# Kernel optimization log

Hardware: AMD Instinct MI355X
Metric: run time of the kernel (lower is better)

Reference implementation:

```python
import jax, jax.numpy as jnp
import numpy as np

NUM_HEADS = 16


def setup_inputs() -> dict:
    key = jax.random.key(0)
    ks = jax.random.split(key, 6)
    B, S, E = 2, 2048, 1024
    scale = 1.0 / np.sqrt(E)
    return {
        "x": jax.random.normal(ks[0], (B, S, E), dtype=jnp.float32),
        "mask": jnp.ones((B, S), dtype=jnp.int32),
        "Wq": jax.random.normal(ks[1], (E, E), dtype=jnp.float32) * scale,
        "bq": jnp.zeros((E,), dtype=jnp.float32),
        "Wk": jax.random.normal(ks[2], (E, E), dtype=jnp.float32) * scale,
        "bk": jnp.zeros((E,), dtype=jnp.float32),
        "Wv": jax.random.normal(ks[3], (E, E), dtype=jnp.float32) * scale,
        "bv": jnp.zeros((E,), dtype=jnp.float32),
        "Wo": jax.random.normal(ks[4], (E, E), dtype=jnp.float32) * scale,
        "bo": jnp.zeros((E,), dtype=jnp.float32),
    }


def reference(x, mask, Wq, bq, Wk, bk, Wv, bv, Wo, bo):
    B, S, E = x.shape
    H = NUM_HEADS
    D = E // H

    def heads(t):  # [B,S,E] -> [B,H,S,D]
        return t.reshape(B, S, H, D).transpose(0, 2, 1, 3)

    q = heads(x @ Wq + bq)
    k = heads(x @ Wk + bk)
    v = heads(x @ Wv + bv)

    # scaled dot-product scores [B,H,S,S]
    scores = jnp.einsum("bhsd,bhtd->bhst", q, k) / jnp.sqrt(jnp.float32(D))
    m = mask.astype(jnp.float32)[:, None, None, :]  # key-side padding mask
    scores = scores + (-1e9) * (1.0 - m)
    weights = jax.nn.softmax(scores, axis=-1)
    attn = jnp.einsum("bhst,bhtd->bhsd", weights, v)

    concat = attn.transpose(0, 2, 1, 3).reshape(B, S, E)
    return concat @ Wo + bo
```

## Files before the change

kernel.cpp:

```cpp
#include <hip/hip_runtime.h>
#include <stdint.h>

#define E_DIM   1024
#define HNUM    16
#define DH      64
#define BATCH   2
#define SEQ     2048
#define M_TOT   (BATCH*SEQ)
#define LOG2E   1.44269504088896340736f

typedef __bf16 bf16x8 __attribute__((ext_vector_type(8)));
typedef __bf16 bf16x4 __attribute__((ext_vector_type(4)));
typedef float  f32x4  __attribute__((ext_vector_type(4)));
typedef float  f32x16 __attribute__((ext_vector_type(16)));
typedef unsigned short u16;
typedef unsigned int   u32;
typedef unsigned long long u64;
typedef u16 u16x8 __attribute__((ext_vector_type(8)));
typedef u32 u32x2 __attribute__((ext_vector_type(2)));

__device__ __forceinline__ u16 f2bf(float f) {
    u32 u = __builtin_bit_cast(u32, f);
    u32 r = 0x7FFFu + ((u >> 16) & 1u);
    return (u16)((u + r) >> 16);
}

__device__ __forceinline__ void gload_lds16(const u16* g, u16* l) {
    __builtin_amdgcn_global_load_lds(
        (const __attribute__((address_space(1))) u32*)g,
        (__attribute__((address_space(3))) u32*)l, 16, 0, 0);
}

#define MFMA16(a,b,c) __builtin_amdgcn_mfma_f32_16x16x32_bf16((a),(b),(c),0,0,0)
#define MFMA32(a,b,c) __builtin_amdgcn_mfma_f32_32x32x16_bf16((a),(b),(c),0,0,0)

__global__ __launch_bounds__(256) void cast_x_kernel(const float* __restrict__ x,
                                                     u16* __restrict__ out, int n) {
    int idx = (blockIdx.x * 256 + threadIdx.x) * 4;
    if (idx < n) {
        float4 v = *reinterpret_cast<const float4*>(x + idx);
        ushort4 o;
        o.x = f2bf(v.x); o.y = f2bf(v.y); o.z = f2bf(v.z); o.w = f2bf(v.w);
        *reinterpret_cast<ushort4*>(out + idx) = o;
    }
}

__global__ __launch_bounds__(256) void maskbits_kernel(const int* __restrict__ mask,
                                                       u64* __restrict__ bits) {
    int i = blockIdx.x * 256 + threadIdx.x;
    u64 bl = __ballot(mask[i] != 0);
    if ((i & 63) == 0) bits[i >> 6] = bl;
}

__global__ void wtrans_kernel(const float* __restrict__ w0, const float* __restrict__ w1,
                              const float* __restrict__ w2, const float* __restrict__ w3,
                              u16* __restrict__ out) {
    __shared__ float tile[32][33];
    const float* w = blockIdx.z == 0 ? w0 : blockIdx.z == 1 ? w1 : blockIdx.z == 2 ? w2 : w3;
    const int n0 = blockIdx.x * 32, k0 = blockIdx.y * 32;
    #pragma unroll
    for (int j = 0; j < 4; j++) {
        int k = k0 + threadIdx.y + j * 8;
        tile[threadIdx.y + j * 8][threadIdx.x] = w[(size_t)k * E_DIM + n0 + threadIdx.x];
    }
    __syncthreads();
    u16* o = out + (size_t)blockIdx.z * E_DIM * E_DIM;
    #pragma unroll
    for (int j = 0; j < 4; j++) {
        int n = n0 + threadIdx.y + j * 8;
        o[(size_t)n * E_DIM + k0 + threadIdx.x] = f2bf(tile[threadIdx.x][threadIdx.y + j * 8]);
    }
}

template <typename OutT>
__global__ __launch_bounds__(256) void gemm_kernel(
    const u16* __restrict__ A, const u16* __restrict__ Bt_base, OutT* __restrict__ C_base,
    const float* __restrict__ bias0, const float* __restrict__ bias1,
    const float* __restrict__ bias2, float scale0, int Mdim) {
    const int z = blockIdx.z;
    const u16* Bt = Bt_base + (size_t)z * E_DIM * E_DIM;
    OutT* C = C_base + (size_t)z * Mdim * E_DIM;
    const float* bias = (z == 0) ? bias0 : (z == 1 ? bias1 : bias2);
    const float scale = (z == 0) ? scale0 : 1.0f;

    __shared__ __align__(16) u16 Als[128 * 32];
    __shared__ __align__(16) u16 Bls[128 * 32];

    const int tid = threadIdx.x;
    const int lane = tid & 63;
    const int w = tid >> 6;
    const int wr = (w >> 1) * 64, wc = (w & 1) * 64;
    const int tm = blockIdx.y * 128, tn = blockIdx.x * 128;
    const int r4 = tid >> 2;
    const int c8 = (tid & 3) * 8;

    f32x4 acc[4][4] = {};

    for (int k0 = 0; k0 < E_DIM; k0 += 32) {
        gload_lds16(A + (size_t)(tm + r4) * E_DIM + k0 + c8, Als + tid * 8);
        gload_lds16(A + (size_t)(tm + 64 + r4) * E_DIM + k0 + c8, Als + 2048 + tid * 8);
        gload_lds16(Bt + (size_t)(tn + r4) * E_DIM + k0 + c8, Bls + tid * 8);
        gload_lds16(Bt + (size_t)(tn + 64 + r4) * E_DIM + k0 + c8, Bls + 2048 + tid * 8);
        __syncthreads();
        const int lr = lane & 15, lg = lane >> 4;
        bf16x8 af[4], bfr[4];
        #pragma unroll
        for (int m = 0; m < 4; m++)
            af[m] = *reinterpret_cast<const bf16x8*>(Als + (wr + m * 16 + lr) * 32 + lg * 8);
        #pragma unroll
        for (int n = 0; n < 4; n++)
            bfr[n] = *reinterpret_cast<const bf16x8*>(Bls + (wc + n * 16 + lr) * 32 + lg * 8);
        #pragma unroll
        for (int m = 0; m < 4; m++)
            #pragma unroll
            for (int n = 0; n < 4; n++)
                acc[m][n] = MFMA16(af[m], bfr[n], acc[m][n]);
        __syncthreads();
    }

    const int lr = lane & 15, lg = lane >> 4;
    #pragma unroll
    for (int m = 0; m < 4; m++) {
        #pragma unroll
        for (int n = 0; n < 4; n++) {
            const int col = tn + wc + n * 16 + lr;
            const float bv = bias[col];
            #pragma unroll
            for (int r = 0; r < 4; r++) {
                const int row = tm + wr + m * 16 + lg * 4 + r;
                float v = (acc[m][n][r] + bv) * scale;
                if constexpr (sizeof(OutT) == 2) {
                    C[(size_t)row * E_DIM + col] = f2bf(v);
                } else {
                    C[(size_t)row * E_DIM + col] = v;
                }
            }
        }
    }
}

__global__ __launch_bounds__(256) void attn_kernel(
    const u16* __restrict__ Q, const u16* __restrict__ K, const u16* __restrict__ V,
    const u64* __restrict__ mbits, u16* __restrict__ PO, float* __restrict__ lws) {
    __shared__ __align__(16) u16 Kls[4][64 * 64];
    __shared__ __align__(16) u16 Vt[2][64 * 64];

    const int tid = threadIdx.x;
    const int lane = tid & 63;
    const int w = tid >> 6;
    const int hi = lane >> 5;
    const int l31 = lane & 31;
    const int n = blockIdx.x;
    const int g = n & 63, qt = n >> 6;
    const int h = g & 15, zz = g >> 4;
    const int b = zz >> 1, half = zz & 1;

    const int qrow = b * SEQ + qt * 128 + w * 32 + l31;
    bf16x8 qf[4];
    #pragma unroll
    for (int kc = 0; kc < 4; kc++)
        qf[kc] = *reinterpret_cast<const bf16x8*>(Q + (size_t)qrow * E_DIM + h * DH + kc * 16 + hi * 8);

    const int krow = (l31 & 3) | ((l31 & 4) << 1) | ((l31 & 8) >> 1) | (l31 & 16);
    const u32 ksw = (u32)(krow & 7) << 4;

    const int krA = tid >> 3;
    const int kcA = (tid & 7) ^ (krA & 7);
    const size_t kgoffA = (size_t)krA * E_DIM + kcA * 8;
    const size_t kgoffB = kgoffA + (size_t)32 * E_DIM;

    const int vc = tid & 7;
    const int vsg = ((tid >> 3) ^ (vc << 2)) & 31;
    const size_t vgoff = (size_t)(2 * vsg) * E_DIM + vc * 8;

    f32x16 oacc0 = {}, oacc1 = {};
    float l_run = 0.f;

    const u16* Kg = K + (size_t)(b * SEQ + half * (SEQ / 2)) * E_DIM + h * DH;
    const u16* Vg = V + (size_t)(b * SEQ + half * (SEQ / 2)) * E_DIM + h * DH;
    const int NT = SEQ / 2 / 64;

    {
        u16x8 a0 = __builtin_bit_cast(u16x8, *reinterpret_cast<const bf16x8*>(Vg + vgoff));
        u16x8 a1 = __builtin_bit_cast(u16x8, *reinterpret_cast<const bf16x8*>(Vg + vgoff + E_DIM));
        gload_lds16(Kg + kgoffA, &Kls[0][tid * 8]);
        gload_lds16(Kg + kgoffB, &Kls[0][(tid + 256) * 8]);
        gload_lds16(Kg + (size_t)64 * E_DIM + kgoffA, &Kls[1][tid * 8]);
        gload_lds16(Kg + (size_t)64 * E_DIM + kgoffB, &Kls[1][(tid + 256) * 8]);
        #pragma unroll
        for (int j = 0; j < 8; j++) {
            const u32 off = (((u32)(vc * 8 + j) * 128) + (u32)vsg * 4) ^ ((u32)j << 4);
            *(u32*)((char*)Vt[0] + off) = (u32)a0[j] | ((u32)a1[j] << 16);
        }
        asm volatile("s_waitcnt vmcnt(2)" ::: "memory");
        asm volatile("s_waitcnt lgkmcnt(0)" ::: "memory");
        __builtin_amdgcn_sched_barrier(0);
        __builtin_amdgcn_s_barrier();
    }

    for (int kt = 0; kt < NT; kt++) {
        u16x8 a0, a1;
        if (kt + 1 < NT) {
            const u16* vg = Vg + (size_t)(kt + 1) * 64 * E_DIM;
            a0 = __builtin_bit_cast(u16x8, *reinterpret_cast<const bf16x8*>(vg + vgoff));
            a1 = __builtin_bit_cast(u16x8, *reinterpret_cast<const bf16x8*>(vg + vgoff + E_DIM));
        }
        if (kt + 2 < NT) {
            const u16* kg = Kg + (size_t)(kt + 2) * 64 * E_DIM;
            gload_lds16(kg + kgoffA, &Kls[(kt + 2) & 3][tid * 8]);
            gload_lds16(kg + kgoffB, &Kls[(kt + 2) & 3][(tid + 256) * 8]);
        }

        const char* Kb = (const char*)Kls[kt & 3];
        const char* Vb = (const char*)Vt[kt & 1];
        const u64 mb = mbits[b * (SEQ / 64) + half * NT + kt];
        float sum = 0.f;

        #pragma unroll
        for (int kh = 0; kh < 2; kh++) {
            f32x16 s = {};
            __builtin_amdgcn_s_setprio(1);
            #pragma unroll
            for (int kc = 0; kc < 4; kc++) {
                const u32 off = ((((u32)krow * 128) + (u32)kc * 32 + (u32)hi * 16) ^ ksw)
                                + (u32)kh * 4096;
                bf16x8 kf = *(const bf16x8*)(Kb + off);
                s = MFMA32(kf, qf[kc], s);
            }
            __builtin_amdgcn_s_setprio(0);
            if (mb != ~0ull) {
                #pragma unroll
                for (int r = 0; r < 16; r++) {
                    const int key = 32 * kh + (r & 3) + 4 * ((r >> 2) & 1) + 8 * hi
                                    + 16 * ((r >> 3) & 1);
                    if (!((mb >> key) & 1)) s[r] += -1.442695e9f;
                }
            }
            #pragma unroll
            for (int r = 0; r < 16; r++) { s[r] = exp2f(s[r]); sum += s[r]; }
            bf16x8 pf0, pf1;
            #pragma unroll
            for (int e = 0; e < 8; e++) { pf0[e] = (__bf16)s[e]; pf1[e] = (__bf16)s[8 + e]; }
            __builtin_amdgcn_s_setprio(1);
            #pragma unroll
            for (int kp = 0; kp < 2; kp++) {
                const int kc = 2 * kh + kp;
                const u32 roff = (((u32)l31 * 128) + (u32)(2 * kc + hi) * 16)
                                 ^ ((u32)(l31 & 7) << 4);
                bf16x8 vf0 = *(const bf16x8*)(Vb + roff);
                bf16x8 vf1 = *(const bf16x8*)(Vb + roff + 4096);
                const bf16x8 pfx = kp ? pf1 : pf0;
                oacc0 = MFMA32(vf0, pfx, oacc0);
                oacc1 = MFMA32(vf1, pfx, oacc1);
            }
            __builtin_amdgcn_s_setprio(0);
        }
        l_run += sum;

        asm volatile("s_waitcnt vmcnt(2)" ::: "memory");
        __builtin_amdgcn_sched_barrier(0);
        if (kt + 1 < NT) {
            #pragma unroll
            for (int j = 0; j < 8; j++) {
                const u32 off = (((u32)(vc * 8 + j) * 128) + (u32)vsg * 4) ^ ((u32)j << 4);
                *(u32*)((char*)Vt[(kt + 1) & 1] + off) = (u32)a0[j] | ((u32)a1[j] << 16);
            }
        }
        asm volatile("s_waitcnt lgkmcnt(0)" ::: "memory");
        __builtin_amdgcn_sched_barrier(0);
        __builtin_amdgcn_s_barrier();
    }

    const float l_tot = l_run + __shfl_xor(l_run, 32);
    u16* op = PO + ((size_t)half * M_TOT + qrow) * E_DIM + h * DH;
    #pragma unroll
    for (int db = 0; db < 2; db++) {
        #pragma unroll
        for (int j = 0; j < 4; j++) {
            bf16x4 pk;
            #pragma unroll
            for (int c = 0; c < 4; c++)
                pk[c] = (__bf16)(db ? oacc1[4 * j + c] : oacc0[4 * j + c]);
            const int d0 = 32 * db + 8 * j + 4 * hi;
            *reinterpret_cast<u32x2*>(op + d0) = __builtin_bit_cast(u32x2, pk);
        }
    }
    if (hi == 0) lws[((size_t)half * M_TOT + qrow) * HNUM + h] = l_tot;
}

__global__ __launch_bounds__(256) void combine_kernel(const u16* __restrict__ PO,
                                                      const float* __restrict__ lws,
                                                      u16* __restrict__ ab) {
    const int i = (blockIdx.x * 256 + threadIdx.x) * 8;
    const int row = i >> 10;
    const int h = (i & 1023) >> 6;
    const float l0 = lws[(size_t)row * HNUM + h];
    const float l1 = lws[((size_t)M_TOT + row) * HNUM + h];
    const float rl = 1.0f / (l0 + l1);
    const bf16x8 a = *reinterpret_cast<const bf16x8*>(PO + i);
    const bf16x8 c = *reinterpret_cast<const bf16x8*>(PO + (size_t)M_TOT * E_DIM + i);
    u16x8 o;
    #pragma unroll
    for (int j = 0; j < 8; j++)
        o[j] = f2bf(((float)a[j] + (float)c[j]) * rl);
    *reinterpret_cast<u16x8*>(ab + i) = o;
}

extern "C" void kernel_launch(void* const* d_in, const int* in_sizes, int n_in,
                              void* d_out, int out_size, void* d_ws, size_t ws_size,
                              hipStream_t stream) {
    const float* x  = (const float*)d_in[0];
    const int* mask = (const int*)d_in[1];
    const float* Wq = (const float*)d_in[2];
    const float* bq = (const float*)d_in[3];
    const float* Wk = (const float*)d_in[4];
    const float* bk = (const float*)d_in[5];
    const float* Wv = (const float*)d_in[6];
    const float* bv = (const float*)d_in[7];
    const float* Wo = (const float*)d_in[8];
    const float* bo = (const float*)d_in[9];
    float* out = (float*)d_out;

    u16* ws  = (u16*)d_ws;
    const size_t ME = (size_t)M_TOT * E_DIM;
    u16* xb  = ws;
    u16* wt  = ws + ME;
    u16* qb  = ws + 2 * ME;
    u16* kbf = ws + 3 * ME;
    u16* vbf = ws + 4 * ME;
    u64* mbf = (u64*)(ws + 5 * ME);
    float* lws = (float*)(ws + 5 * ME + 8192);
    u16* ab  = xb;
    u16* po  = (u16*)d_out;

    cast_x_kernel<<<dim3(M_TOT * E_DIM / 1024), dim3(256), 0, stream>>>(x, xb, M_TOT * E_DIM);
    wtrans_kernel<<<dim3(E_DIM / 32, E_DIM / 32, 4), dim3(32, 8), 0, stream>>>(Wq, Wk, Wv, Wo, wt);
    maskbits_kernel<<<dim3(M_TOT / 256), dim3(256), 0, stream>>>(mask, mbf);
    gemm_kernel<u16><<<dim3(E_DIM / 128, M_TOT / 128, 3), dim3(256), 0, stream>>>(
        xb, wt, qb, bq, bk, bv, 0.125f * LOG2E, M_TOT);
    attn_kernel<<<dim3(1024), dim3(256), 0, stream>>>(qb, kbf, vbf, mbf, po, lws);
    combine_kernel<<<dim3(M_TOT * E_DIM / 2048), dim3(256), 0, stream>>>(po, lws, ab);
    gemm_kernel<float><<<dim3(E_DIM / 128, M_TOT / 128, 1), dim3(256), 0, stream>>>(
        ab, wt + (size_t)3 * E_DIM * E_DIM, out, bo, bo, bo, 1.0f, M_TOT);
}
```

Before: 150.5 us.

## Software-pipeline QK^T one tile ahead and deepen K prefetch in attention

Restructures the attention loop so the QK^T MFMAs for the next key tile are issued while softmax exp and PV MFMAs for the current tile run. This overlaps the exp/convert latency with matrix work. K prefetch depth grows from two to three tiles ahead. The change also precomputes the LDS offsets, uses the v_cvt_pk_bf16_f32 packed conversion and the raw exp2 builtin, and transposes V with perm instructions. The cost is higher register pressure from the extra score accumulators.

```diff
diff --git a/kernel.cpp b/kernel.cpp
--- a/kernel.cpp
+++ b/kernel.cpp
@@ -18,6 +18,7 @@
 typedef unsigned long long u64;
 typedef u16 u16x8 __attribute__((ext_vector_type(8)));
 typedef u32 u32x2 __attribute__((ext_vector_type(2)));
+typedef u32 u32x4 __attribute__((ext_vector_type(4)));
 
 __device__ __forceinline__ u16 f2bf(float f) {
     u32 u = __builtin_bit_cast(u32, f);
@@ -29,6 +30,12 @@
     __builtin_amdgcn_global_load_lds(
         (const __attribute__((address_space(1))) u32*)g,
         (__attribute__((address_space(3))) u32*)l, 16, 0, 0);
+}
+
+__device__ __forceinline__ u32 cvt_pk_bf16(float lo, float hi) {
+    u32 r;
+    asm("v_cvt_pk_bf16_f32 %0, %1, %2" : "=v"(r) : "v"(lo), "v"(hi));
+    return r;
 }
 
 #define MFMA16(a,b,c) __builtin_amdgcn_mfma_f32_16x16x32_bf16((a),(b),(c),0,0,0)
@@ -163,6 +170,10 @@
 
     const int krow = (l31 & 3) | ((l31 & 4) << 1) | ((l31 & 8) >> 1) | (l31 & 16);
     const u32 ksw = (u32)(krow & 7) << 4;
+    u32 koff[4];
+    #pragma unroll
+    for (int kc = 0; kc < 4; kc++)
+        koff[kc] = (((u32)krow * 128) + (u32)kc * 32 + (u32)hi * 16) ^ ksw;
 
     const int krA = tid >> 3;
     const int kcA = (tid & 7) ^ (krA & 7);
@@ -172,103 +183,152 @@
     const int vc = tid & 7;
     const int vsg = ((tid >> 3) ^ (vc << 2)) & 31;
     const size_t vgoff = (size_t)(2 * vsg) * E_DIM + vc * 8;
+    u32 vwoff[8];
+    #pragma unroll
+    for (int j = 0; j < 8; j++)
+        vwoff[j] = (((u32)(vc * 8 + j) * 128) + (u32)vsg * 4) ^ ((u32)j << 4);
+    u32 vroff[4];
+    #pragma unroll
+    for (int kc = 0; kc < 4; kc++)
+        vroff[kc] = (((u32)l31 * 128) + (u32)(2 * kc + hi) * 16) ^ (((u32)(l31 & 7)) << 4);
 
     f32x16 oacc0 = {}, oacc1 = {};
     float l_run = 0.f;
 
     const u16* Kg = K + (size_t)(b * SEQ + half * (SEQ / 2)) * E_DIM + h * DH;
     const u16* Vg = V + (size_t)(b * SEQ + half * (SEQ / 2)) * E_DIM + h * DH;
+    const size_t TSTEP = (size_t)64 * E_DIM;
+    const u16* kga = Kg + kgoffA;
+    const u16* kgb = Kg + kgoffB;
+    const u16* vgp = Vg + vgoff;
     const int NT = SEQ / 2 / 64;
 
     {
-        u16x8 a0 = __builtin_bit_cast(u16x8, *reinterpret_cast<const bf16x8*>(Vg + vgoff));
-        u16x8 a1 = __builtin_bit_cast(u16x8, *reinterpret_cast<const bf16x8*>(Vg + vgoff + E_DIM));
-        gload_lds16(Kg + kgoffA, &Kls[0][tid * 8]);
-        gload_lds16(Kg + kgoffB, &Kls[0][(tid + 256) * 8]);
-        gload_lds16(Kg + (size_t)64 * E_DIM + kgoffA, &Kls[1][tid * 8]);
-        gload_lds16(Kg + (size_t)64 * E_DIM + kgoffB, &Kls[1][(tid + 256) * 8]);
-        #pragma unroll
-        for (int j = 0; j < 8; j++) {
-            const u32 off = (((u32)(vc * 8 + j) * 128) + (u32)vsg * 4) ^ ((u32)j << 4);
-            *(u32*)((char*)Vt[0] + off) = (u32)a0[j] | ((u32)a1[j] << 16);
-        }
+        u32x4 a0 = *reinterpret_cast<const u32x4*>(vgp);
+        u32x4 a1 = *reinterpret_cast<const u32x4*>(vgp + E_DIM);
+        gload_lds16(kga,             &Kls[0][tid * 8]);
+        gload_lds16(kgb,             &Kls[0][(tid + 256) * 8]);
+        gload_lds16(kga + TSTEP,     &Kls[1][tid * 8]);
+        gload_lds16(kgb + TSTEP,     &Kls[1][(tid + 256) * 8]);
+        gload_lds16(kga + 2 * TSTEP, &Kls[2][tid * 8]);
+        gload_lds16(kgb + 2 * TSTEP, &Kls[2][(tid + 256) * 8]);
+        kga += 3 * TSTEP; kgb += 3 * TSTEP; vgp += TSTEP;
         asm volatile("s_waitcnt vmcnt(2)" ::: "memory");
+        __builtin_amdgcn_sched_barrier(0);
+        #pragma unroll
+        for (int j = 0; j < 8; j++)
+            *(u32*)((char*)Vt + vwoff[j]) = __builtin_amdgcn_perm(
+                a1[j >> 1], a0[j >> 1], (j & 1) ? 0x07060302u : 0x05040100u);
         asm volatile("s_waitcnt lgkmcnt(0)" ::: "memory");
         __builtin_amdgcn_sched_barrier(0);
         __builtin_amdgcn_s_barrier();
     }
 
-    for (int kt = 0; kt < NT; kt++) {
-        u16x8 a0, a1;
-        if (kt + 1 < NT) {
-            const u16* vg = Vg + (size_t)(kt + 1) * 64 * E_DIM;
-            a0 = __builtin_bit_cast(u16x8, *reinterpret_cast<const bf16x8*>(vg + vgoff));
-            a1 = __builtin_bit_cast(u16x8, *reinterpret_cast<const bf16x8*>(vg + vgoff + E_DIM));
-        }
-        if (kt + 2 < NT) {
-            const u16* kg = Kg + (size_t)(kt + 2) * 64 * E_DIM;
-            gload_lds16(kg + kgoffA, &Kls[(kt + 2) & 3][tid * 8]);
-            gload_lds16(kg + kgoffB, &Kls[(kt + 2) & 3][(tid + 256) * 8]);
-        }
-
-        const char* Kb = (const char*)Kls[kt & 3];
-        const char* Vb = (const char*)Vt[kt & 1];
-        const u64 mb = mbits[b * (SEQ / 64) + half * NT + kt];
+    f32x16 sc0 = {}, sc1 = {};
+    {
+        const char* Kb = (const char*)Kls;
+        __builtin_amdgcn_s_setprio(1);
+        #pragma unroll
+        for (int kc = 0; kc < 4; kc++) {
+            bf16x8 kf0 = *(const bf16x8*)(Kb + koff[kc]);
+            bf16x8 kf1 = *(const bf16x8*)(Kb + koff[kc] + 4096);
+            sc0 = MFMA32(kf0, qf[kc], sc0);
+            sc1 = MFMA32(kf1, qf[kc], sc1);
+        }
+        __builtin_amdgcn_s_setprio(0);
+    }
+
+    for (int t = 0; t < NT; t++) {
+        const bool haveV = (t + 1 < NT);
+        const bool haveK = (t + 3 < NT);
+        u32x4 a0, a1;
+        if (haveV) {
+            a0 = *reinterpret_cast<const u32x4*>(vgp);
+            a1 = *reinterpret_cast<const u32x4*>(vgp + E_DIM);
+        }
+        if (haveK) {
+            gload_lds16(kga, &Kls[(t + 3) & 3][tid * 8]);
+            gload_lds16(kgb, &Kls[(t + 3) & 3][(tid + 256) * 8]);
+        }
+
+        const u64 mb = mbits[b * (SEQ / 64) + half * NT + t];
+        if (mb != ~0ull) {
+            #pragma unroll
+            for (int r = 0; r < 16; r++) {
+                const int key = (r & 3) + 4 * ((r >> 2) & 1) + 8 * hi + 16 * ((r >> 3) & 1);
+                if (!((mb >> key) & 1))        sc0[r] += -1.442695e9f;
+                if (!((mb >> (32 + key)) & 1)) sc1[r] += -1.442695e9f;
+            }
+        }
         float sum = 0.f;
-
-        #pragma unroll
-        for (int kh = 0; kh < 2; kh++) {
-            f32x16 s = {};
+        #pragma unroll
+        for (int r = 0; r < 16; r++) {
+            sc0[r] = __builtin_amdgcn_exp2f(sc0[r]); sum += sc0[r];
+        }
+        #pragma unroll
+        for (int r = 0; r < 16; r++) {
+            sc1[r] = __builtin_amdgcn_exp2f(sc1[r]); sum += sc1[r];
+        }
+        l_run += sum;
+
+        bf16x8 pf[4];
+        {
+            u32x4 pw0, pw1, pw2, pw3;
+            #pragma unroll
+            for (int e = 0; e < 4; e++) {
+                pw0[e] = cvt_pk_bf16(sc0[2 * e],     sc0[2 * e + 1]);
+                pw1[e] = cvt_pk_bf16(sc0[8 + 2 * e], sc0[9 + 2 * e]);
+                pw2[e] = cvt_pk_bf16(sc1[2 * e],     sc1[2 * e + 1]);
+                pw3[e] = cvt_pk_bf16(sc1[8 + 2 * e], sc1[9 + 2 * e]);
+            }
+            pf[0] = __builtin_bit_cast(bf16x8, pw0);
+            pf[1] = __builtin_bit_cast(bf16x8, pw1);
+            pf[2] = __builtin_bit_cast(bf16x8, pw2);
+            pf[3] = __builtin_bit_cast(bf16x8, pw3);
+        }
+
+        f32x16 sn0 = {}, sn1 = {};
+        if (haveV) {
+            const char* Kb = (const char*)Kls + ((t + 1) & 3) * 8192;
             __builtin_amdgcn_s_setprio(1);
             #pragma unroll
             for (int kc = 0; kc < 4; kc++) {
-                const u32 off = ((((u32)krow * 128) + (u32)kc * 32 + (u32)hi * 16) ^ ksw)
-                                + (u32)kh * 4096;
-                bf16x8 kf = *(const bf16x8*)(Kb + off);
-                s = MFMA32(kf, qf[kc], s);
+                bf16x8 kf0 = *(const bf16x8*)(Kb + koff[kc]);
+                bf16x8 kf1 = *(const bf16x8*)(Kb + koff[kc] + 4096);
+                sn0 = MFMA32(kf0, qf[kc], sn0);
+                sn1 = MFMA32(kf1, qf[kc], sn1);
             }
             __builtin_amdgcn_s_setprio(0);
-            if (mb != ~0ull) {
-                #pragma unroll
-                for (int r = 0; r < 16; r++) {
-                    const int key = 32 * kh + (r & 3) + 4 * ((r >> 2) & 1) + 8 * hi
-                                    + 16 * ((r >> 3) & 1);
-                    if (!((mb >> key) & 1)) s[r] += -1.442695e9f;
-                }
-            }
-            #pragma unroll
-            for (int r = 0; r < 16; r++) { s[r] = exp2f(s[r]); sum += s[r]; }
-            bf16x8 pf0, pf1;
-            #pragma unroll
-            for (int e = 0; e < 8; e++) { pf0[e] = (__bf16)s[e]; pf1[e] = (__bf16)s[8 + e]; }
+        }
+
+        {
+            const char* Vb = (const char*)Vt + (t & 1) * 8192;
             __builtin_amdgcn_s_setprio(1);
             #pragma unroll
-            for (int kp = 0; kp < 2; kp++) {
-                const int kc = 2 * kh + kp;
-                const u32 roff = (((u32)l31 * 128) + (u32)(2 * kc + hi) * 16)
-                                 ^ ((u32)(l31 & 7) << 4);
-                bf16x8 vf0 = *(const bf16x8*)(Vb + roff);
-                bf16x8 vf1 = *(const bf16x8*)(Vb + roff + 4096);
-                const bf16x8 pfx = kp ? pf1 : pf0;
-                oacc0 = MFMA32(vf0, pfx, oacc0);
-                oacc1 = MFMA32(vf1, pfx, oacc1);
+            for (int kc = 0; kc < 4; kc++) {
+                bf16x8 vf0 = *(const bf16x8*)(Vb + vroff[kc]);
+                bf16x8 vf1 = *(const bf16x8*)(Vb + vroff[kc] + 4096);
+                oacc0 = MFMA32(vf0, pf[kc], oacc0);
+                oacc1 = MFMA32(vf1, pf[kc], oacc1);
             }
             __builtin_amdgcn_s_setprio(0);
         }
-        l_run += sum;
 
         asm volatile("s_waitcnt vmcnt(2)" ::: "memory");
         __builtin_amdgcn_sched_barrier(0);
-        if (kt + 1 < NT) {
-            #pragma unroll
-            for (int j = 0; j < 8; j++) {
-                const u32 off = (((u32)(vc * 8 + j) * 128) + (u32)vsg * 4) ^ ((u32)j << 4);
-                *(u32*)((char*)Vt[(kt + 1) & 1] + off) = (u32)a0[j] | ((u32)a1[j] << 16);
-            }
+        if (haveV) {
+            #pragma unroll
+            for (int j = 0; j < 8; j++)
+                *(u32*)((char*)Vt + ((t + 1) & 1) * 8192 + vwoff[j]) = __builtin_amdgcn_perm(
+                    a1[j >> 1], a0[j >> 1], (j & 1) ? 0x07060302u : 0x05040100u);
         }
         asm volatile("s_waitcnt lgkmcnt(0)" ::: "memory");
         __builtin_amdgcn_sched_barrier(0);
         __builtin_amdgcn_s_barrier();
+
+        sc0 = sn0; sc1 = sn1;
+        if (haveK) { kga += TSTEP; kgb += TSTEP; }
+        if (haveV) { vgp += TSTEP; }
     }
 
     const float l_tot = l_run + __shfl_xor(l_run, 32);
@@ -277,12 +337,13 @@
     for (int db = 0; db < 2; db++) {
         #pragma unroll
         for (int j = 0; j < 4; j++) {
-            bf16x4 pk;
-            #pragma unroll
-            for (int c = 0; c < 4; c++)
-                pk[c] = (__bf16)(db ? oacc1[4 * j + c] : oacc0[4 * j + c]);
+            u32x2 pk;
+            pk[0] = cvt_pk_bf16(db ? oacc1[4 * j + 0] : oacc0[4 * j + 0],
+                                db ? oacc1[4 * j + 1] : oacc0[4 * j + 1]);
+            pk[1] = cvt_pk_bf16(db ? oacc1[4 * j + 2] : oacc0[4 * j + 2],
+                                db ? oacc1[4 * j + 3] : oacc0[4 * j + 3]);
             const int d0 = 32 * db + 8 * j + 4 * hi;
-            *reinterpret_cast<u32x2*>(op + d0) = __builtin_bit_cast(u32x2, pk);
+            *reinterpret_cast<u32x2*>(op + d0) = pk;
         }
     }
     if (hi == 0) lws[((size_t)half * M_TOT + qrow) * HNUM + h] = l_tot;
```

Result: faster. 133.8 us (-11.1%).
